# Optimization experiments

Hardware: AMD Instinct MI355X
Metric: run time of the kernel (lower is better)

Reference implementation:

```python
import jax, jax.numpy as jnp
import numpy as np

IN_SIZE = 512
HID = 512
BATCH = 65536


def setup_inputs() -> dict:
    key = jax.random.key(0)
    ks = jax.random.split(key, 20)
    s = 1.0 / np.sqrt(IN_SIZE)
    sh = 1.0 / np.sqrt(HID)
    d = {
        "inputs": jax.random.normal(ks[0], (BATCH, IN_SIZE), jnp.float32),
        "state": jax.random.normal(ks[1], (BATCH, HID), jnp.float32),
        "parent_state": jax.random.normal(ks[2], (BATCH, HID), jnp.float32),
    }
    # input-path linears (with bias), torch Linear layout: W [out, in], y = x @ W.T + b
    for i, name in enumerate(["w_a", "w_r", "w_r1", "w_c"]):
        d[name + "_w"] = jax.random.uniform(ks[3 + 2 * i], (HID, IN_SIZE), jnp.float32, -s, s)
        d[name + "_b"] = jax.random.uniform(ks[4 + 2 * i], (HID,), jnp.float32, -s, s)
    # state-path and parent-path linears (no bias)
    for i, name in enumerate(["u_a", "u_r", "u_r1", "u_c", "p_a", "p_r", "p_r1", "p_c"]):
        d[name + "_w"] = jax.random.uniform(ks[11 + i], (HID, HID), jnp.float32, -sh, sh)
    return d


def reference(inputs, state, parent_state,
              w_a_w, w_a_b, w_r_w, w_r_b, w_r1_w, w_r1_b, w_c_w, w_c_b,
              u_a_w, u_r_w, u_r1_w, u_c_w,
              p_a_w, p_r_w, p_r1_w, p_c_w):
    def lin(x, w, b=None):
        y = x @ w.T
        return y if b is None else y + b

    att = jax.nn.sigmoid(lin(inputs, w_a_w, w_a_b) + lin(state, u_a_w) + lin(parent_state, p_a_w))
    r = jax.nn.sigmoid(lin(inputs, w_r_w, w_r_b) + lin(state, u_r_w) + lin(parent_state, p_r_w))
    r1 = jax.nn.sigmoid(lin(inputs, w_r1_w, w_r1_b) + lin(state, u_r1_w) + lin(parent_state, p_r1_w))
    c = jnp.tanh(lin(inputs, w_c_w, w_c_b) + lin(state * r, u_c_w) + lin(parent_state * r1, p_c_w))
    new_h = att * c + (1.0 - att) * state
    return new_h
```

## Files before the change

kernel.cpp:

```cpp
#include <hip/hip_runtime.h>
#include <stdint.h>


typedef unsigned short u16;
using bf16x8 = __attribute__((ext_vector_type(8))) __bf16;
using f32x4  = __attribute__((ext_vector_type(4))) float;

__device__ __forceinline__ u16 f2bf(float f) {
    __bf16 b = (__bf16)f;
    union { __bf16 b; u16 u; } v; v.b = b;
    return v.u;
}
__device__ __forceinline__ uint32_t f2bf2(float lo, float hi) {
    return (uint32_t)f2bf(lo) | ((uint32_t)f2bf(hi) << 16);
}
__device__ __forceinline__ float bf2f(u16 s) {
    union { uint32_t u; float f; } v; v.u = ((uint32_t)s) << 16;
    return v.f;
}
__device__ __forceinline__ void load_lds16(const void* g, void* l) {
    __builtin_amdgcn_global_load_lds(
        (const __attribute__((address_space(1))) uint32_t*)g,
        (__attribute__((address_space(3))) uint32_t*)l, 16, 0, 0);
}
__device__ __forceinline__ void fence_bar() {
    asm volatile("" ::: "memory");
    __builtin_amdgcn_s_barrier();
    asm volatile("" ::: "memory");
}

__global__ void prep_weights(
    const float* __restrict__ wa, const float* __restrict__ ua, const float* __restrict__ pa,
    const float* __restrict__ wrg, const float* __restrict__ ur, const float* __restrict__ pr,
    const float* __restrict__ wr1, const float* __restrict__ ur1, const float* __restrict__ pr1,
    const float* __restrict__ wcc, const float* __restrict__ uc, const float* __restrict__ pc,
    u16* __restrict__ B1, u16* __restrict__ B2)
{
    int idx = blockIdx.x * 256 + threadIdx.x;
    const int T1 = 1536 * 1536;
    if (idx < T1) {
        int n = idx / 1536, k = idx - n * 1536;
        int g = n >> 9, nn = n & 511;
        int o = k >> 9, kk = k & 511;
        const float* s;
        if (g == 0)      s = (o == 0) ? wa  : (o == 1) ? ua  : pa;
        else if (g == 1) s = (o == 0) ? wrg : (o == 1) ? ur  : pr;
        else             s = (o == 0) ? wr1 : (o == 1) ? ur1 : pr1;
        B1[idx] = f2bf(s[nn * 512 + kk]);
    } else {
        int j = idx - T1;
        if (j < 512 * 1536) {
            int n = j / 1536, k = j - n * 1536;
            int o = k >> 9, kk = k & 511;
            const float* s = (o == 0) ? wcc : (o == 1) ? uc : pc;
            B2[j] = f2bf(s[n * 512 + kk]);
        }
    }
}

__global__ void cast_inputs(const float* __restrict__ X, const float* __restrict__ H,
                            const float* __restrict__ P,
                            u16* __restrict__ Xb, u16* __restrict__ Hb, u16* __restrict__ Pb)
{
    const long long MAT8 = (65536LL * 512) / 8;
    for (long long t = (long long)blockIdx.x * 256 + threadIdx.x;
         t < 3 * MAT8; t += (long long)gridDim.x * 256) {
        int m = (int)(t >> 22);
        long long e = (t & (MAT8 - 1)) * 8;
        const float* s = (m == 0) ? X : (m == 1) ? H : P;
        u16* d = (m == 0) ? Xb : (m == 1) ? Hb : Pb;
        f32x4 a = *(const f32x4*)(s + e);
        f32x4 b = *(const f32x4*)(s + e + 4);
        uint4 q;
        q.x = f2bf2(a.x, a.y); q.y = f2bf2(a.z, a.w);
        q.z = f2bf2(b.x, b.y); q.w = f2bf2(b.z, b.w);
        *(uint4*)(d + e) = q;
    }
}

template<int MODE>
__global__ __launch_bounds__(512, 2)
void gemm256(const u16* __restrict__ A0, const u16* __restrict__ A1s, const u16* __restrict__ A2s,
             const u16* __restrict__ Bw,
             const float* __restrict__ bias0, const float* __restrict__ bias1,
             const float* __restrict__ bias2,
             const u16* __restrict__ HbP, const u16* __restrict__ PbP,
             const float* __restrict__ Hf,
             float* __restrict__ outp, u16* __restrict__ hrw, u16* __restrict__ pr1w)
{
    __shared__ u16 lds[65536];
    constexpr int NT = 24;

    const int tid  = threadIdx.x;
    const int lane = tid & 63;
    const int wv   = tid >> 6;
    const int wr   = wv >> 2;
    const int wc   = wv & 3;

    int panel, ntl;
    const int xcd = blockIdx.x & 7;
    const int idx = blockIdx.x >> 3;
    if (MODE == 1) { panel = xcd * 32 + idx / 6;    ntl = idx % 6; }
    else           { panel = xcd * 32 + (idx >> 1); ntl = idx & 1; }
    const int m0 = panel * 256;
    const int n0 = ntl * 256;

    const int srow = tid >> 3;
    const int scg  = ((tid & 7) ^ (srow & 7)) * 8;
    const int ldst = srow * 64 + (tid & 7) * 8;

    const int fr = lane & 15;
    const int fk = (lane >> 4) * 8;
    const int sw = (lane & 7) * 8;

    f32x4 acc[8][4];
    const f32x4 vzero = {0.0f, 0.0f, 0.0f, 0.0f};
#pragma unroll
    for (int i = 0; i < 8; ++i)
#pragma unroll
        for (int j = 0; j < 4; ++j) acc[i][j] = vzero;

    auto stageA = [&](int T, int h) {
        const u16* src = (T < 8) ? A0 : (T < 16) ? A1s : A2s;
        const u16* g = src + (size_t)(m0 + h * 128 + srow) * 512 + (T & 7) * 64 + scg;
        u16* lb = &lds[(T & 1) * 32768 + h * 8192 + ldst];
        load_lds16(g, lb);
        load_lds16(g + (size_t)64 * 512, lb + 4096);
    };
    auto stageB = [&](int T, int h) {
        const u16* g = Bw + (size_t)(n0 + h * 128 + srow) * 1536 + T * 64 + scg;
        u16* lb = &lds[(T & 1) * 32768 + 16384 + h * 8192 + ldst];
        load_lds16(g, lb);
        load_lds16(g + (size_t)64 * 1536, lb + 4096);
    };

    stageA(0, 0); stageA(0, 1);
    stageB(0, 0); stageB(0, 1);
    stageB(1, 0); stageB(1, 1);
    asm volatile("s_waitcnt vmcnt(4)" ::: "memory");
    fence_bar();

    for (int T = 0; T < NT; ++T) {
        const int cb = (T & 1) * 32768;
        bf16x8 bF[4][2];
#pragma unroll
        for (int q = 0; q < 4; ++q) {
            if (q == 0) {
#pragma unroll
                for (int j = 0; j < 4; ++j)
#pragma unroll
                    for (int ks = 0; ks < 2; ++ks)
                        bF[j][ks] = *(const bf16x8*)&lds[cb + 16384
                            + (wc * 64 + j * 16 + fr) * 64 + ((ks * 32 + fk) ^ sw)];
            }
            bf16x8 aF[2][2];
#pragma unroll
            for (int i = 0; i < 2; ++i)
#pragma unroll
                for (int ks = 0; ks < 2; ++ks)
                    aF[i][ks] = *(const bf16x8*)&lds[cb
                        + (wr * 128 + (q * 2 + i) * 16 + fr) * 64 + ((ks * 32 + fk) ^ sw)];

            if (q == 0) { if (T < NT - 1) stageA(T + 1, 0); }
            if (q == 1) { if (T < NT - 1) stageA(T + 1, 1);
                          if (T < NT - 2) stageB(T + 2, 0); }
            if (q == 2) { if (T < NT - 2) stageB(T + 2, 1); }

            fence_bar();
            asm volatile("s_waitcnt lgkmcnt(0)" ::: "memory");
            __builtin_amdgcn_sched_barrier(0);
            __builtin_amdgcn_s_setprio(1);
#pragma unroll
            for (int i = 0; i < 2; ++i)
#pragma unroll
                for (int j = 0; j < 4; ++j)
#pragma unroll
                    for (int ks = 0; ks < 2; ++ks)
                        acc[q * 2 + i][j] = __builtin_amdgcn_mfma_f32_16x16x32_bf16(
                            aF[i][ks], bF[j][ks], acc[q * 2 + i][j], 0, 0, 0);
            __builtin_amdgcn_s_setprio(0);
            if (q == 3) {
                if (T < NT - 2)       asm volatile("s_waitcnt vmcnt(4)" ::: "memory");
                else if (T == NT - 2) asm volatile("s_waitcnt vmcnt(0)" ::: "memory");
            }
            fence_bar();
        }
    }

    const int rbase = m0 + wr * 128 + (lane >> 4) * 4;
    if (MODE == 1) {
        const int g = ntl >> 1;
        const float* bias = (g == 0) ? bias0 : (g == 1) ? bias1 : bias2;
        const int ncb = (ntl & 1) * 256 + wc * 64;
#pragma unroll
        for (int i = 0; i < 8; ++i)
#pragma unroll
            for (int j = 0; j < 4; ++j) {
                const int nn = ncb + j * 16 + fr;
                const float b = bias[nn];
#pragma unroll
                for (int jj = 0; jj < 4; ++jj) {
                    const int row = rbase + i * 16 + jj;
                    const size_t off = (size_t)row * 512 + nn;
                    float v = acc[i][j][jj] + b;
                    float s = 1.0f / (1.0f + __expf(-v));
                    if (g == 0)      outp[off] = s;
                    else if (g == 1) hrw[off]  = f2bf(s * bf2f(HbP[off]));
                    else             pr1w[off] = f2bf(s * bf2f(PbP[off]));
                }
            }
    } else {
        const int ncb = n0 + wc * 64;
#pragma unroll
        for (int i = 0; i < 8; ++i)
#pragma unroll
            for (int j = 0; j < 4; ++j) {
                const int nn = ncb + j * 16 + fr;
                const float b = bias0[nn];
#pragma unroll
                for (int jj = 0; jj < 4; ++jj) {
                    const int row = rbase + i * 16 + jj;
                    const size_t off = (size_t)row * 512 + nn;
                    float v = acc[i][j][jj] + b;
                    float e = __expf(2.0f * v);
                    float ct = 1.0f - 2.0f / (e + 1.0f);
                    float a = outp[off];
                    outp[off] = a * ct + (1.0f - a) * Hf[off];
                }
            }
    }
}

__global__ __launch_bounds__(256, 2)
void k1_small(const float* __restrict__ X, const float* __restrict__ H,
              const float* __restrict__ P, const u16* __restrict__ B1,
              const float* __restrict__ ba, const float* __restrict__ br,
              const float* __restrict__ br1,
              float* __restrict__ attf, u16* __restrict__ hrw, u16* __restrict__ pr1w)
{
    __shared__ u16 Ab[2][128 * 64];
    __shared__ u16 Bb[2][128 * 64];
    const int tid = threadIdx.x, lane = tid & 63, w = tid >> 6;
    const int wr = w >> 1, wc = w & 1;
    const int bid = blockIdx.x, xcd = bid & 7, idx = bid >> 3;
    const int panel = idx / 12, ntl = idx - panel * 12;
    const int m0 = (xcd * 64 + panel) * 128, n0 = ntl * 128;
    const int srow = w * 32 + (lane >> 3);
    const int scol = ((lane & 7) ^ (lane >> 3)) * 8;
    const int arow = tid >> 4, acol = (tid & 15) * 4;
    const int aswz = acol ^ ((arow & 7) << 3);
    f32x4 acc[4][4];
    const f32x4 vz = {0, 0, 0, 0};
#pragma unroll
    for (int i = 0; i < 4; ++i)
#pragma unroll
        for (int j = 0; j < 4; ++j) acc[i][j] = vz;
    f32x4 areg[8];
    auto issueA = [&](int kt) {
        const float* src = (kt < 8) ? X : (kt < 16) ? H : P;
        const float* base = src + (size_t)(m0 + arow) * 512 + (kt & 7) * 64 + acol;
#pragma unroll
        for (int rr = 0; rr < 8; ++rr)
            areg[rr] = *(const f32x4*)(base + (size_t)(rr * 16) * 512);
    };
    auto writeA = [&](int nb) {
#pragma unroll
        for (int rr = 0; rr < 8; ++rr) {
            uint2 q; q.x = f2bf2(areg[rr].x, areg[rr].y);
            q.y = f2bf2(areg[rr].z, areg[rr].w);
            *(uint2*)&Ab[nb][(arow + rr * 16) * 64 + aswz] = q;
        }
    };
    auto issueB = [&](int kt, int nb) {
        const u16* gb = B1 + (size_t)(n0 + srow) * 1536 + kt * 64 + scol;
        u16* lb = &Bb[nb][(w * 32) * 64];
#pragma unroll
        for (int c = 0; c < 4; ++c)
            load_lds16(gb + (size_t)c * 8 * 1536, lb + c * 8 * 64);
    };
    auto compute = [&](int cb) {
        const int rsw = (lane & 7) << 3, rb = lane & 15, hi8 = (lane >> 4) * 8;
#pragma unroll
        for (int ks = 0; ks < 2; ++ks) {
            bf16x8 af[4], bfr[4];
            const int col = (ks * 32 + hi8) ^ rsw;
#pragma unroll
            for (int fm = 0; fm < 4; ++fm)
                af[fm] = *(const bf16x8*)&Ab[cb][(wr * 64 + fm * 16 + rb) * 64 + col];
#pragma unroll
            for (int fn = 0; fn < 4; ++fn)
                bfr[fn] = *(const bf16x8*)&Bb[cb][(wc * 64 + fn * 16 + rb) * 64 + col];
#pragma unroll
            for (int fm = 0; fm < 4; ++fm)
#pragma unroll
                for (int fn = 0; fn < 4; ++fn)
                    acc[fm][fn] = __builtin_amdgcn_mfma_f32_16x16x32_bf16(
                        af[fm], bfr[fn], acc[fm][fn], 0, 0, 0);
        }
    };
    issueA(0); issueB(0, 0); writeA(0);
    __syncthreads();
    int cb = 0;
#pragma unroll 2
    for (int kt = 0; kt < 24; ++kt) {
        if (kt < 23) { issueA(kt + 1); issueB(kt + 1, cb ^ 1); }
        compute(cb);
        if (kt < 23) writeA(cb ^ 1);
        __syncthreads();
        cb ^= 1;
    }
    const int gate = ntl >> 2;
    const float* bias = (gate == 0) ? ba : (gate == 1) ? br : br1;
    const int nnb = (ntl & 3) * 128 + wc * 64;
    const int rl = (lane >> 4) * 4, cl = lane & 15;
#pragma unroll
    for (int fm = 0; fm < 4; ++fm)
#pragma unroll
        for (int fn = 0; fn < 4; ++fn) {
            const int nn = nnb + fn * 16 + cl;
            const float b = bias[nn];
#pragma unroll
            for (int j = 0; j < 4; ++j) {
                const int row = m0 + wr * 64 + fm * 16 + rl + j;
                const size_t off = (size_t)row * 512 + nn;
                float v = acc[fm][fn][j] + b;
                float s = 1.0f / (1.0f + __expf(-v));
                if (gate == 0)      attf[off] = s;
                else if (gate == 1) hrw[off]  = f2bf(s * H[off]);
                else                pr1w[off] = f2bf(s * P[off]);
            }
        }
}

__global__ __launch_bounds__(256, 2)
void k2_small(const float* __restrict__ X, const float* __restrict__ H,
              const u16* __restrict__ B2, const float* __restrict__ bc,
              const u16* __restrict__ hrw, const u16* __restrict__ pr1w,
              float* outp)
{
    __shared__ u16 Ab[2][128 * 64];
    __shared__ u16 Bb[2][128 * 64];
    const int tid = threadIdx.x, lane = tid & 63, w = tid >> 6;
    const int wr = w >> 1, wc = w & 1;
    const int bid = blockIdx.x, xcd = bid & 7, idx = bid >> 3;
    const int panel = idx >> 2, ntl = idx & 3;
    const int m0 = (xcd * 64 + panel) * 128, n0 = ntl * 128;
    const int srow = w * 32 + (lane >> 3);
    const int scol = ((lane & 7) ^ (lane >> 3)) * 8;
    const int arow = tid >> 4, acol = (tid & 15) * 4;
    const int aswz = acol ^ ((arow & 7) << 3);
    f32x4 acc[4][4];
    const f32x4 vz = {0, 0, 0, 0};
#pragma unroll
    for (int i = 0; i < 4; ++i)
#pragma unroll
        for (int j = 0; j < 4; ++j) acc[i][j] = vz;
    f32x4 areg[8];
    auto issueA = [&](int kt, int nb) {
        if (kt >= 8) {
            const u16* src = (kt < 16) ? hrw : pr1w;
            const u16* gb = src + (size_t)(m0 + srow) * 512 + (kt & 7) * 64 + scol;
            u16* lb = &Ab[nb][(w * 32) * 64];
#pragma unroll
            for (int c = 0; c < 4; ++c)
                load_lds16(gb + (size_t)c * 8 * 512, lb + c * 8 * 64);
        } else {
            const float* base = X + (size_t)(m0 + arow) * 512 + (kt & 7) * 64 + acol;
#pragma unroll
            for (int rr = 0; rr < 8; ++rr)
                areg[rr] = *(const f32x4*)(base + (size_t)(rr * 16) * 512);
        }
    };
    auto writeA = [&](int kt, int nb) {
        if (kt < 8) {
#pragma unroll
            for (int rr = 0; rr < 8; ++rr) {
                uint2 q; q.x = f2bf2(areg[rr].x, areg[rr].y);
                q.y = f2bf2(areg[rr].z, areg[rr].w);
                *(uint2*)&Ab[nb][(arow + rr * 16) * 64 + aswz] = q;
            }
        }
    };
    auto issueB = [&](int kt, int nb) {
        const u16* gb = B2 + (size_t)(n0 + srow) * 1536 + kt * 64 + scol;
        u16* lb = &Bb[nb][(w * 32) * 64];
#pragma unroll
        for (int c = 0; c < 4; ++c)
            load_lds16(gb + (size_t)c * 8 * 1536, lb + c * 8 * 64);
    };
    auto compute = [&](int cb) {
        const int rsw = (lane & 7) << 3, rb = lane & 15, hi8 = (lane >> 4) * 8;
#pragma unroll
        for (int ks = 0; ks < 2; ++ks) {
            bf16x8 af[4], bfr[4];
            const int col = (ks * 32 + hi8) ^ rsw;
#pragma unroll
            for (int fm = 0; fm < 4; ++fm)
                af[fm] = *(const bf16x8*)&Ab[cb][(wr * 64 + fm * 16 + rb) * 64 + col];
#pragma unroll
            for (int fn = 0; fn < 4; ++fn)
                bfr[fn] = *(const bf16x8*)&Bb[cb][(wc * 64 + fn * 16 + rb) * 64 + col];
#pragma unroll
            for (int fm = 0; fm < 4; ++fm)
#pragma unroll
                for (int fn = 0; fn < 4; ++fn)
                    acc[fm][fn] = __builtin_amdgcn_mfma_f32_16x16x32_bf16(
                        af[fm], bfr[fn], acc[fm][fn], 0, 0, 0);
        }
    };
    issueA(0, 0); issueB(0, 0); writeA(0, 0);
    __syncthreads();
    int cb = 0;
#pragma unroll 2
    for (int kt = 0; kt < 24; ++kt) {
        if (kt < 23) { issueA(kt + 1, cb ^ 1); issueB(kt + 1, cb ^ 1); }
        compute(cb);
        if (kt < 23) writeA(kt + 1, cb ^ 1);
        __syncthreads();
        cb ^= 1;
    }
    const int nnb = n0 + wc * 64;
    const int rl = (lane >> 4) * 4, cl = lane & 15;
#pragma unroll
    for (int fm = 0; fm < 4; ++fm)
#pragma unroll
        for (int fn = 0; fn < 4; ++fn) {
            const int nn = nnb + fn * 16 + cl;
            const float b = bc[nn];
#pragma unroll
            for (int j = 0; j < 4; ++j) {
                const int row = m0 + wr * 64 + fm * 16 + rl + j;
                const size_t off = (size_t)row * 512 + nn;
                float v = acc[fm][fn][j] + b;
                float e = __expf(2.0f * v);
                float ct = 1.0f - 2.0f / (e + 1.0f);
                float a = outp[off];
                outp[off] = a * ct + (1.0f - a) * H[off];
            }
        }
}

extern "C" void kernel_launch(void* const* d_in, const int* in_sizes, int n_in,
                              void* d_out, int out_size, void* d_ws, size_t ws_size,
                              hipStream_t stream)
{
    const float* X   = (const float*)d_in[0];
    const float* H   = (const float*)d_in[1];
    const float* P   = (const float*)d_in[2];
    const float* wa  = (const float*)d_in[3];
    const float* ba  = (const float*)d_in[4];
    const float* wrg = (const float*)d_in[5];
    const float* br  = (const float*)d_in[6];
    const float* wr1 = (const float*)d_in[7];
    const float* br1 = (const float*)d_in[8];
    const float* wcc = (const float*)d_in[9];
    const float* bc  = (const float*)d_in[10];
    const float* ua  = (const float*)d_in[11];
    const float* ur  = (const float*)d_in[12];
    const float* ur1 = (const float*)d_in[13];
    const float* uc  = (const float*)d_in[14];
    const float* pa  = (const float*)d_in[15];
    const float* pr  = (const float*)d_in[16];
    const float* pr1 = (const float*)d_in[17];
    const float* pc  = (const float*)d_in[18];

    char* ws = (char*)d_ws;
    u16* B1   = (u16*)(ws);
    u16* B2   = (u16*)(ws + (size_t)4718592);
    u16* hrp  = (u16*)(ws + (size_t)6291456);
    u16* pr1p = (u16*)(ws + (size_t)73400320);
    u16* Xb   = (u16*)(ws + (size_t)140509184);
    u16* Hb   = (u16*)(ws + (size_t)207618048);
    u16* Pb   = (u16*)(ws + (size_t)274726912);
    float* out = (float*)d_out;

    const bool big = ws_size >= (size_t)341835776ULL;

    prep_weights<<<12288, 256, 0, stream>>>(wa, ua, pa, wrg, ur, pr, wr1, ur1, pr1,
                                            wcc, uc, pc, B1, B2);
    if (big) {
        cast_inputs<<<3072, 256, 0, stream>>>(X, H, P, Xb, Hb, Pb);
        gemm256<1><<<1536, 512, 0, stream>>>(Xb, Hb, Pb, B1, ba, br, br1,
                                             Hb, Pb, nullptr, out, hrp, pr1p);
        gemm256<2><<<512, 512, 0, stream>>>(Xb, hrp, pr1p, B2, bc, nullptr, nullptr,
                                            nullptr, nullptr, H, out, nullptr, nullptr);
    } else {
        k1_small<<<6144, 256, 0, stream>>>(X, H, P, B1, ba, br, br1, out, hrp, pr1p);
        k2_small<<<2048, 256, 0, stream>>>(X, H, B2, bc, hrp, pr1p, out);
    }
}
```

Measured before the change: 752.1 us.

## Replace 256x256 GEMM with 128x128 double-buffered tiles and bf16 attention buffer

```diff
diff --git a/kernel.cpp b/kernel.cpp
--- a/kernel.cpp
+++ b/kernel.cpp
@@ -22,11 +22,6 @@
     __builtin_amdgcn_global_load_lds(
         (const __attribute__((address_space(1))) uint32_t*)g,
         (__attribute__((address_space(3))) uint32_t*)l, 16, 0, 0);
-}
-__device__ __forceinline__ void fence_bar() {
-    asm volatile("" ::: "memory");
-    __builtin_amdgcn_s_barrier();
-    asm volatile("" ::: "memory");
 }
 
 __global__ void prep_weights(
@@ -78,154 +73,144 @@
     }
 }
 
-template<int MODE>
-__global__ __launch_bounds__(512, 2)
-void gemm256(const u16* __restrict__ A0, const u16* __restrict__ A1s, const u16* __restrict__ A2s,
-             const u16* __restrict__ Bw,
-             const float* __restrict__ bias0, const float* __restrict__ bias1,
-             const float* __restrict__ bias2,
-             const u16* __restrict__ HbP, const u16* __restrict__ PbP,
-             const float* __restrict__ Hf,
-             float* __restrict__ outp, u16* __restrict__ hrw, u16* __restrict__ pr1w)
-{
-    __shared__ u16 lds[65536];
-    constexpr int NT = 24;
+template<int MODE, bool ATTB>
+__global__ __launch_bounds__(256, 2)
+void g128(const u16* __restrict__ A0, const u16* __restrict__ A1s, const u16* __restrict__ A2s,
+          const u16* __restrict__ Bw,
+          const float* __restrict__ bias0, const float* __restrict__ bias1,
+          const float* __restrict__ bias2,
+          const u16* __restrict__ HbP, const u16* __restrict__ PbP,
+          u16* __restrict__ attb, u16* __restrict__ hrw, u16* __restrict__ pr1w,
+          float* __restrict__ outp)
+{
+    __shared__ u16 Ab[2][128 * 64];
+    __shared__ u16 Bb[2][128 * 64];
 
     const int tid  = threadIdx.x;
     const int lane = tid & 63;
-    const int wv   = tid >> 6;
-    const int wr   = wv >> 2;
-    const int wc   = wv & 3;
+    const int w    = tid >> 6;
+    const int wr   = w >> 1;
+    const int wc   = w & 1;
 
     int panel, ntl;
     const int xcd = blockIdx.x & 7;
     const int idx = blockIdx.x >> 3;
-    if (MODE == 1) { panel = xcd * 32 + idx / 6;    ntl = idx % 6; }
-    else           { panel = xcd * 32 + (idx >> 1); ntl = idx & 1; }
-    const int m0 = panel * 256;
-    const int n0 = ntl * 256;
-
-    const int srow = tid >> 3;
-    const int scg  = ((tid & 7) ^ (srow & 7)) * 8;
-    const int ldst = srow * 64 + (tid & 7) * 8;
-
-    const int fr = lane & 15;
-    const int fk = (lane >> 4) * 8;
-    const int sw = (lane & 7) * 8;
-
-    f32x4 acc[8][4];
-    const f32x4 vzero = {0.0f, 0.0f, 0.0f, 0.0f};
-#pragma unroll
-    for (int i = 0; i < 8; ++i)
-#pragma unroll
-        for (int j = 0; j < 4; ++j) acc[i][j] = vzero;
-
-    auto stageA = [&](int T, int h) {
-        const u16* src = (T < 8) ? A0 : (T < 16) ? A1s : A2s;
-        const u16* g = src + (size_t)(m0 + h * 128 + srow) * 512 + (T & 7) * 64 + scg;
-        u16* lb = &lds[(T & 1) * 32768 + h * 8192 + ldst];
-        load_lds16(g, lb);
-        load_lds16(g + (size_t)64 * 512, lb + 4096);
-    };
-    auto stageB = [&](int T, int h) {
-        const u16* g = Bw + (size_t)(n0 + h * 128 + srow) * 1536 + T * 64 + scg;
-        u16* lb = &lds[(T & 1) * 32768 + 16384 + h * 8192 + ldst];
-        load_lds16(g, lb);
-        load_lds16(g + (size_t)64 * 1536, lb + 4096);
-    };
-
-    stageA(0, 0); stageA(0, 1);
-    stageB(0, 0); stageB(0, 1);
-    stageB(1, 0); stageB(1, 1);
-    asm volatile("s_waitcnt vmcnt(4)" ::: "memory");
-    fence_bar();
-
-    for (int T = 0; T < NT; ++T) {
-        const int cb = (T & 1) * 32768;
-        bf16x8 bF[4][2];
-#pragma unroll
-        for (int q = 0; q < 4; ++q) {
-            if (q == 0) {
-#pragma unroll
-                for (int j = 0; j < 4; ++j)
-#pragma unroll
-                    for (int ks = 0; ks < 2; ++ks)
-                        bF[j][ks] = *(const bf16x8*)&lds[cb + 16384
-                            + (wc * 64 + j * 16 + fr) * 64 + ((ks * 32 + fk) ^ sw)];
-            }
-            bf16x8 aF[2][2];
-#pragma unroll
-            for (int i = 0; i < 2; ++i)
-#pragma unroll
-                for (int ks = 0; ks < 2; ++ks)
-                    aF[i][ks] = *(const bf16x8*)&lds[cb
-                        + (wr * 128 + (q * 2 + i) * 16 + fr) * 64 + ((ks * 32 + fk) ^ sw)];
-
-            if (q == 0) { if (T < NT - 1) stageA(T + 1, 0); }
-            if (q == 1) { if (T < NT - 1) stageA(T + 1, 1);
-                          if (T < NT - 2) stageB(T + 2, 0); }
-            if (q == 2) { if (T < NT - 2) stageB(T + 2, 1); }
-
-            fence_bar();
-            asm volatile("s_waitcnt lgkmcnt(0)" ::: "memory");
-            __builtin_amdgcn_sched_barrier(0);
-            __builtin_amdgcn_s_setprio(1);
-#pragma unroll
-            for (int i = 0; i < 2; ++i)
-#pragma unroll
-                for (int j = 0; j < 4; ++j)
-#pragma unroll
-                    for (int ks = 0; ks < 2; ++ks)
-                        acc[q * 2 + i][j] = __builtin_amdgcn_mfma_f32_16x16x32_bf16(
-                            aF[i][ks], bF[j][ks], acc[q * 2 + i][j], 0, 0, 0);
-            __builtin_amdgcn_s_setprio(0);
-            if (q == 3) {
-                if (T < NT - 2)       asm volatile("s_waitcnt vmcnt(4)" ::: "memory");
-                else if (T == NT - 2) asm volatile("s_waitcnt vmcnt(0)" ::: "memory");
-            }
-            fence_bar();
-        }
-    }
-
-    const int rbase = m0 + wr * 128 + (lane >> 4) * 4;
+    if (MODE == 1) { panel = xcd * 64 + idx / 12;   ntl = idx % 12; }
+    else           { panel = xcd * 64 + (idx >> 2); ntl = idx & 3;  }
+    const int m0 = panel * 128;
+    const int n0 = ntl * 128;
+
+    const int srow = w * 32 + (lane >> 3);
+    const int scol = ((lane & 7) ^ (lane >> 3)) * 8;
+    const int ofsA = srow * 512  + scol;
+    const int ofsB = srow * 1536 + scol;
+    const u16* const bA0 = A0  + (size_t)m0 * 512;
+    const u16* const bA1 = A1s + (size_t)m0 * 512;
+    const u16* const bA2 = A2s + (size_t)m0 * 512;
+    const u16* const bB  = Bw  + (size_t)n0 * 1536;
+
+    auto issueA = [&](int kt, int nb) {
+        const u16* src = (kt < 8) ? bA0 : (kt < 16) ? bA1 : bA2;
+        const u16* g = src + (kt & 7) * 64 + ofsA;
+        u16* lb = &Ab[nb][(w * 32) * 64];
+#pragma unroll
+        for (int c = 0; c < 4; ++c)
+            load_lds16(g + c * 8 * 512, lb + c * 8 * 64);
+    };
+    auto issueB = [&](int kt, int nb) {
+        const u16* g = bB + kt * 64 + ofsB;
+        u16* lb = &Bb[nb][(w * 32) * 64];
+#pragma unroll
+        for (int c = 0; c < 4; ++c)
+            load_lds16(g + c * 8 * 1536, lb + c * 8 * 64);
+    };
+
+    f32x4 acc[4][4];
+    const f32x4 vz = {0.0f, 0.0f, 0.0f, 0.0f};
+#pragma unroll
+    for (int i = 0; i < 4; ++i)
+#pragma unroll
+        for (int j = 0; j < 4; ++j) acc[i][j] = vz;
+
+    auto compute = [&](int cb) {
+        const int rsw = (lane & 7) << 3;
+        const int rb  = lane & 15;
+        const int hi8 = (lane >> 4) * 8;
+#pragma unroll
+        for (int ks = 0; ks < 2; ++ks) {
+            bf16x8 af[4], bfr[4];
+            const int col = (ks * 32 + hi8) ^ rsw;
+#pragma unroll
+            for (int fm = 0; fm < 4; ++fm)
+                af[fm] = *(const bf16x8*)&Ab[cb][(wr * 64 + fm * 16 + rb) * 64 + col];
+#pragma unroll
+            for (int fn = 0; fn < 4; ++fn)
+                bfr[fn] = *(const bf16x8*)&Bb[cb][(wc * 64 + fn * 16 + rb) * 64 + col];
+#pragma unroll
+            for (int fm = 0; fm < 4; ++fm)
+#pragma unroll
+                for (int fn = 0; fn < 4; ++fn)
+                    acc[fm][fn] = __builtin_amdgcn_mfma_f32_16x16x32_bf16(
+                        af[fm], bfr[fn], acc[fm][fn], 0, 0, 0);
+        }
+    };
+
+    issueA(0, 0); issueB(0, 0);
+    __syncthreads();
+    int cb = 0;
+#pragma unroll 1
+    for (int kt = 0; kt < 24; ++kt) {
+        if (kt < 23) { issueA(kt + 1, cb ^ 1); issueB(kt + 1, cb ^ 1); }
+        compute(cb);
+        __syncthreads();
+        cb ^= 1;
+    }
+
+    const int rl = (lane >> 4) * 4;
+    const int cl = lane & 15;
+    const int rb0 = m0 + wr * 64 + rl;
     if (MODE == 1) {
-        const int g = ntl >> 1;
-        const float* bias = (g == 0) ? bias0 : (g == 1) ? bias1 : bias2;
-        const int ncb = (ntl & 1) * 256 + wc * 64;
-#pragma unroll
-        for (int i = 0; i < 8; ++i)
-#pragma unroll
-            for (int j = 0; j < 4; ++j) {
-                const int nn = ncb + j * 16 + fr;
+        const int gate = ntl >> 2;
+        const float* bias = (gate == 0) ? bias0 : (gate == 1) ? bias1 : bias2;
+        const int nnb = (ntl & 3) * 128 + wc * 64;
+#pragma unroll
+        for (int fm = 0; fm < 4; ++fm)
+#pragma unroll
+            for (int fn = 0; fn < 4; ++fn) {
+                const int nn = nnb + fn * 16 + cl;
                 const float b = bias[nn];
-#pragma unroll
-                for (int jj = 0; jj < 4; ++jj) {
-                    const int row = rbase + i * 16 + jj;
-                    const size_t off = (size_t)row * 512 + nn;
-                    float v = acc[i][j][jj] + b;
+                int off = (rb0 + fm * 16) * 512 + nn;
+#pragma unroll
+                for (int j = 0; j < 4; ++j, off += 512) {
+                    float v = acc[fm][fn][j] + b;
                     float s = 1.0f / (1.0f + __expf(-v));
-                    if (g == 0)      outp[off] = s;
-                    else if (g == 1) hrw[off]  = f2bf(s * bf2f(HbP[off]));
-                    else             pr1w[off] = f2bf(s * bf2f(PbP[off]));
+                    if (gate == 0) {
+                        if (ATTB) attb[off] = f2bf(s);
+                        else      outp[off] = s;
+                    } else if (gate == 1) {
+                        hrw[off]  = f2bf(s * bf2f(HbP[off]));
+                    } else {
+                        pr1w[off] = f2bf(s * bf2f(PbP[off]));
+                    }
                 }
             }
     } else {
-        const int ncb = n0 + wc * 64;
-#pragma unroll
-        for (int i = 0; i < 8; ++i)
-#pragma unroll
-            for (int j = 0; j < 4; ++j) {
-                const int nn = ncb + j * 16 + fr;
+        const int nnb = n0 + wc * 64;
+#pragma unroll
+        for (int fm = 0; fm < 4; ++fm)
+#pragma unroll
+            for (int fn = 0; fn < 4; ++fn) {
+                const int nn = nnb + fn * 16 + cl;
                 const float b = bias0[nn];
-#pragma unroll
-                for (int jj = 0; jj < 4; ++jj) {
-                    const int row = rbase + i * 16 + jj;
-                    const size_t off = (size_t)row * 512 + nn;
-                    float v = acc[i][j][jj] + b;
+                int off = (rb0 + fm * 16) * 512 + nn;
+#pragma unroll
+                for (int j = 0; j < 4; ++j, off += 512) {
+                    float v = acc[fm][fn][j] + b;
                     float e = __expf(2.0f * v);
                     float ct = 1.0f - 2.0f / (e + 1.0f);
-                    float a = outp[off];
-                    outp[off] = a * ct + (1.0f - a) * Hf[off];
+                    float a = ATTB ? bf2f(attb[off]) : outp[off];
+                    float h = bf2f(HbP[off]);
+                    outp[off] = a * ct + (1.0f - a) * h;
                 }
             }
     }
@@ -472,18 +457,27 @@
     u16* Xb   = (u16*)(ws + (size_t)140509184);
     u16* Hb   = (u16*)(ws + (size_t)207618048);
     u16* Pb   = (u16*)(ws + (size_t)274726912);
+    u16* attb = (u16*)(ws + (size_t)341835776);
     float* out = (float*)d_out;
 
-    const bool big = ws_size >= (size_t)341835776ULL;
+    const bool big  = ws_size >= (size_t)341835776ULL;
+    const bool big3 = ws_size >= (size_t)408944640ULL;
 
     prep_weights<<<12288, 256, 0, stream>>>(wa, ua, pa, wrg, ur, pr, wr1, ur1, pr1,
                                             wcc, uc, pc, B1, B2);
     if (big) {
         cast_inputs<<<3072, 256, 0, stream>>>(X, H, P, Xb, Hb, Pb);
-        gemm256<1><<<1536, 512, 0, stream>>>(Xb, Hb, Pb, B1, ba, br, br1,
-                                             Hb, Pb, nullptr, out, hrp, pr1p);
-        gemm256<2><<<512, 512, 0, stream>>>(Xb, hrp, pr1p, B2, bc, nullptr, nullptr,
-                                            nullptr, nullptr, H, out, nullptr, nullptr);
+        if (big3) {
+            g128<1, true><<<6144, 256, 0, stream>>>(Xb, Hb, Pb, B1, ba, br, br1,
+                                                    Hb, Pb, attb, hrp, pr1p, out);
+            g128<2, true><<<2048, 256, 0, stream>>>(Xb, hrp, pr1p, B2, bc, nullptr, nullptr,
+                                                    Hb, nullptr, attb, nullptr, nullptr, out);
+        } else {
+            g128<1, false><<<6144, 256, 0, stream>>>(Xb, Hb, Pb, B1, ba, br, br1,
+                                                     Hb, Pb, nullptr, hrp, pr1p, out);
+            g128<2, false><<<2048, 256, 0, stream>>>(Xb, hrp, pr1p, B2, bc, nullptr, nullptr,
+                                                     Hb, nullptr, nullptr, nullptr, nullptr, out);
+        }
     } else {
         k1_small<<<6144, 256, 0, stream>>>(X, H, P, B1, ba, br, br1, out, hrp, pr1p);
         k2_small<<<2048, 256, 0, stream>>>(X, H, B2, bc, hrp, pr1p, out);
```

Measured after the change: 904.9 us. 1.2x slower.
